# Optimization experiments

Measured on AMD Instinct MI355X. Metric: run time of the kernel, lower is better.

The kernel has to match this reference:

```python
import jax, jax.numpy as jnp
import numpy as np

B, SRC = 32, 1024
SEQ_LEN, CONTEXT_LEN, D_MODEL, VOCAB = 128, 5, 512, 32000


def setup_inputs() -> dict:
    key = jax.random.key(0)
    k1, k2, k3, k4, k5, k6 = jax.random.split(key, 6)
    x = jax.random.randint(k1, (B, SRC), 0, VOCAB, dtype=jnp.int64 if jax.config.jax_enable_x64 else jnp.int32)
    yc = jax.random.randint(k2, (B, SEQ_LEN * CONTEXT_LEN), 0, VOCAB, dtype=x.dtype)
    F_emb = jax.random.normal(k3, (VOCAB, D_MODEL), dtype=jnp.float32) * 0.02
    G_emb = jax.random.normal(k4, (VOCAB, D_MODEL), dtype=jnp.float32) * 0.02
    fan_in = CONTEXT_LEN * D_MODEL
    P_w = jax.random.uniform(k5, (fan_in, D_MODEL), dtype=jnp.float32,
                             minval=-1.0, maxval=1.0) * (fan_in ** -0.5)
    P_b = jnp.zeros((D_MODEL,), dtype=jnp.float32)
    return {"x": x, "yc": yc, "F_emb": F_emb, "G_emb": G_emb, "P_w": P_w, "P_b": P_b}


def reference(x, yc, F_emb, G_emb, P_w, P_b):
    # padding mask from source tokens: 1.0 where token == 0
    mask = (x == 0).astype(jnp.float32)                      # [B, SRC]
    xe = F_emb[x]                                            # [B, SRC, D]
    yce = G_emb[yc].reshape(-1, SEQ_LEN, CONTEXT_LEN * D_MODEL)  # [B, SEQ, C*D]
    py = jnp.einsum('bsk,kd->bsd', yce, P_w) + P_b           # Dense P(y): [B, SEQ, D]
    a = jnp.einsum('bxd,bsd->bxs', xe, py)                   # [B, SRC, SEQ]
    a = a + mask[:, :, None] * -1e9                          # mask padded source rows
    a = jnp.transpose(a, (0, 2, 1))                          # [B, SEQ, SRC]
    a = jax.nn.softmax(a, axis=-1)
    out = jnp.einsum('bsx,bxd->bsd', a, xe)                  # [B, SEQ, D]
    return (out, a)
```

## Files before the change

kernel.cpp:

```cpp
#include <hip/hip_runtime.h>
#include <hip/hip_bf16.h>
#include <stdint.h>

#define BATCH 32
#define SRCN 1024
#define SEQL 128
#define CTXN 5
#define DMOD 512

typedef __attribute__((ext_vector_type(8))) short short8;
typedef __attribute__((ext_vector_type(4))) float floatx4;

typedef __attribute__((address_space(3))) void lds_t;
typedef __attribute__((address_space(1))) void glb_t;

__device__ __forceinline__ void gload_lds16(const void* g, void* l) {
    __builtin_amdgcn_global_load_lds((const glb_t*)g, (lds_t*)l, 16, 0, 0);
}

__device__ __forceinline__ ushort f2b(float f) {
    __hip_bfloat16 h = __float2bfloat16(f);
    return *reinterpret_cast<ushort*>(&h);
}

#define LSLOT(m, sg) ((((m) << 3) | ((sg) ^ ((m) & 7))) << 3)

__global__ __launch_bounds__(256) void k_gather(
    const int* __restrict__ yc, const float* __restrict__ G,
    ushort* __restrict__ yce,
    const float* __restrict__ Pw, ushort* __restrict__ Pwt,
    const int* __restrict__ x, const float* __restrict__ F,
    ushort* __restrict__ xe, ushort* __restrict__ xet)
{
    __shared__ char smem[17408];
    const int tid = threadIdx.x;
    const int bid = blockIdx.x;
    if (bid < 4096) {
        const int r = bid;
        const int b = r >> 7, s = r & 127;
        for (int i = tid; i < 640; i += 256) {
            const int c = i >> 7;
            const int tok = yc[b * (SEQL * CTXN) + s * CTXN + c];
            const float4 v = *(const float4*)(G + (size_t)tok * DMOD + (i & 127) * 4);
            ushort4 o;
            o.x = f2b(v.x); o.y = f2b(v.y); o.z = f2b(v.z); o.w = f2b(v.w);
            *(ushort4*)(yce + (size_t)r * 2560 + i * 4) = o;
        }
    } else if (bid < 4416) {
        float* t = (float*)smem;
        const int id = bid - 4096;
        const int k0 = (id % 40) * 64, n0 = (id / 40) * 64;
        #pragma unroll
        for (int it = 0; it < 4; ++it) {
            const int c = tid + it * 256;
            const int kr = c >> 4, c4 = c & 15;
            const float4 v = *(const float4*)(Pw + (size_t)(k0 + kr) * DMOD + n0 + c4 * 4);
            t[kr * 68 + c4 * 4 + 0] = v.x; t[kr * 68 + c4 * 4 + 1] = v.y;
            t[kr * 68 + c4 * 4 + 2] = v.z; t[kr * 68 + c4 * 4 + 3] = v.w;
        }
        __syncthreads();
        #pragma unroll
        for (int it = 0; it < 2; ++it) {
            const int c = tid + it * 256;
            const int n = c >> 3, seg = c & 7;
            ushort4 o0, o1;
            o0.x = f2b(t[(seg * 8 + 0) * 68 + n]); o0.y = f2b(t[(seg * 8 + 1) * 68 + n]);
            o0.z = f2b(t[(seg * 8 + 2) * 68 + n]); o0.w = f2b(t[(seg * 8 + 3) * 68 + n]);
            o1.x = f2b(t[(seg * 8 + 4) * 68 + n]); o1.y = f2b(t[(seg * 8 + 5) * 68 + n]);
            o1.z = f2b(t[(seg * 8 + 6) * 68 + n]); o1.w = f2b(t[(seg * 8 + 7) * 68 + n]);
            ushort* dst = Pwt + (size_t)(n0 + n) * 2560 + k0 + seg * 8;
            *(ushort4*)dst = o0; *(ushort4*)(dst + 4) = o1;
        }
    } else {
        ushort* t = (ushort*)smem;
        const int id = bid - 4416;
        const int z = id >> 7;
        const int rem = id & 127;
        const int x0 = (rem & 15) * 64, d0 = (rem >> 4) * 64;
        #pragma unroll
        for (int it = 0; it < 4; ++it) {
            const int c = tid + it * 256;
            const int row = c >> 4, seg = c & 15;
            const int tok = x[z * SRCN + x0 + row];
            const float4 v = *(const float4*)(F + (size_t)tok * DMOD + d0 + seg * 4);
            ushort4 o;
            o.x = f2b(v.x); o.y = f2b(v.y); o.z = f2b(v.z); o.w = f2b(v.w);
            *(ushort4*)&t[row * 72 + seg * 4] = o;
            *(ushort4*)(xe + (size_t)(z * SRCN + x0 + row) * DMOD + d0 + seg * 4) = o;
        }
        __syncthreads();
        #pragma unroll
        for (int it = 0; it < 2; ++it) {
            const int c = tid + it * 256;
            const int d = c >> 3, seg = c & 7;
            ushort4 o0, o1;
            o0.x = t[(seg * 8 + 0) * 72 + d]; o0.y = t[(seg * 8 + 1) * 72 + d];
            o0.z = t[(seg * 8 + 2) * 72 + d]; o0.w = t[(seg * 8 + 3) * 72 + d];
            o1.x = t[(seg * 8 + 4) * 72 + d]; o1.y = t[(seg * 8 + 5) * 72 + d];
            o1.z = t[(seg * 8 + 6) * 72 + d]; o1.w = t[(seg * 8 + 7) * 72 + d];
            ushort* dst = xet + (size_t)(z * DMOD + d0 + d) * SRCN + x0 + seg * 8;
            *(ushort4*)dst = o0; *(ushort4*)(dst + 4) = o1;
        }
    }
}

__global__ __launch_bounds__(256) void k_gemm_py(
    const ushort* __restrict__ yce, const ushort* __restrict__ pwt,
    const float* __restrict__ Pb, ushort* __restrict__ py)
{
    __shared__ ushort As[2 * 8 * 512];
    __shared__ ushort Bs[2 * 8 * 512];
    const int f = blockIdx.x;
    const int wg = ((f & 7) << 6) | (f >> 3);
    const int m = wg >> 3, n = wg & 7;
    const int tid = threadIdx.x;
    const int w = tid >> 6, lane = tid & 63;
    const int l15 = lane & 15, q = lane >> 4;
    const int wm = w >> 1, wn = w & 1;
    const int m0 = m * 64, n0 = n * 64;

    const int sr = lane >> 3;
    const int ssg = ((lane & 7) ^ sr) * 8;

    const ushort* Abase = yce + (size_t)(m0 + sr) * 2560 + ssg;
    const ushort* Bbase = pwt + (size_t)(n0 + sr) * 2560 + ssg;

    floatx4 acc[2][2];
    #pragma unroll
    for (int mi = 0; mi < 2; ++mi)
        #pragma unroll
        for (int ni = 0; ni < 2; ++ni)
            acc[mi][ni] = (floatx4){0.f, 0.f, 0.f, 0.f};

    for (int kk = 0; kk < 2560; kk += 128) {
        __syncthreads();
        #pragma unroll
        for (int sub = 0; sub < 2; ++sub) {
            #pragma unroll
            for (int i = 0; i < 2; ++i) {
                const int cc = w * 2 + i;
                gload_lds16(Abase + (size_t)(cc * 8) * 2560 + kk + sub * 64,
                            (void*)(As + sub * 4096 + cc * 512));
                gload_lds16(Bbase + (size_t)(cc * 8) * 2560 + kk + sub * 64,
                            (void*)(Bs + sub * 4096 + cc * 512));
            }
        }
        __syncthreads();
        #pragma unroll
        for (int sub = 0; sub < 2; ++sub) {
            #pragma unroll
            for (int s2 = 0; s2 < 2; ++s2) {
                const int sg = s2 * 4 + q;
                short8 af[2], bf[2];
                #pragma unroll
                for (int mi = 0; mi < 2; ++mi)
                    af[mi] = *(const short8*)(As + sub * 4096 + LSLOT(wm * 32 + mi * 16 + l15, sg));
                #pragma unroll
                for (int ni = 0; ni < 2; ++ni)
                    bf[ni] = *(const short8*)(Bs + sub * 4096 + LSLOT(wn * 32 + ni * 16 + l15, sg));
                #pragma unroll
                for (int mi = 0; mi < 2; ++mi)
                    #pragma unroll
                    for (int ni = 0; ni < 2; ++ni)
                        acc[mi][ni] = __builtin_amdgcn_mfma_f32_16x16x32_bf16(
                            af[mi], bf[ni], acc[mi][ni], 0, 0, 0);
            }
        }
    }

    #pragma unroll
    for (int ni = 0; ni < 2; ++ni) {
        const int col = n0 + wn * 32 + ni * 16 + l15;
        const float bias = Pb[col];
        #pragma unroll
        for (int mi = 0; mi < 2; ++mi) {
            const int row0 = m0 + wm * 32 + mi * 16 + q * 4;
            #pragma unroll
            for (int r = 0; r < 4; ++r)
                py[(size_t)(row0 + r) * DMOD + col] = f2b(acc[mi][ni][r] + bias);
        }
    }
}

__global__ __launch_bounds__(256) void k_gemm_sc(
    const ushort* __restrict__ py, const int* __restrict__ x,
    const ushort* __restrict__ xe, float* __restrict__ a_out)
{
    __shared__ ushort As[16 * 512];
    __shared__ ushort Bs[8 * 512];
    const int f = blockIdx.x;
    const int g = f >> 3;
    const int b = ((g & 3) << 3) | (f & 7);
    const int n = g >> 2;
    const int tid = threadIdx.x;
    const int w = tid >> 6, lane = tid & 63;
    const int l15 = lane & 15, q = lane >> 4;
    const int wm = w >> 1, wn = w & 1;
    const int n0 = n * 64;

    const int sr = lane >> 3;
    const int ssg = ((lane & 7) ^ sr) * 8;

    const ushort* Abase = py + (size_t)(b * SEQL + sr) * DMOD + ssg;
    const ushort* Bbase = xe + (size_t)(b * SRCN + n0 + sr) * DMOD + ssg;

    floatx4 acc[4][2];
    #pragma unroll
    for (int mi = 0; mi < 4; ++mi)
        #pragma unroll
        for (int ni = 0; ni < 2; ++ni)
            acc[mi][ni] = (floatx4){0.f, 0.f, 0.f, 0.f};

    for (int kk = 0; kk < DMOD; kk += 64) {
        __syncthreads();
        #pragma unroll
        for (int i = 0; i < 4; ++i) {
            const int cc = w * 4 + i;
            gload_lds16(Abase + (size_t)(cc * 8) * DMOD + kk, (void*)(As + cc * 512));
        }
        #pragma unroll
        for (int i = 0; i < 2; ++i) {
            const int cc = w * 2 + i;
            gload_lds16(Bbase + (size_t)(cc * 8) * DMOD + kk, (void*)(Bs + cc * 512));
        }
        __syncthreads();
        #pragma unroll
        for (int s2 = 0; s2 < 2; ++s2) {
            const int sg = s2 * 4 + q;
            short8 af[4], bf[2];
            #pragma unroll
            for (int mi = 0; mi < 4; ++mi)
                af[mi] = *(const short8*)(As + LSLOT(wm * 64 + mi * 16 + l15, sg));
            #pragma unroll
            for (int ni = 0; ni < 2; ++ni)
                bf[ni] = *(const short8*)(Bs + LSLOT(wn * 32 + ni * 16 + l15, sg));
            #pragma unroll
            for (int mi = 0; mi < 4; ++mi)
                #pragma unroll
                for (int ni = 0; ni < 2; ++ni)
                    acc[mi][ni] = __builtin_amdgcn_mfma_f32_16x16x32_bf16(
                        af[mi], bf[ni], acc[mi][ni], 0, 0, 0);
        }
    }

    #pragma unroll
    for (int ni = 0; ni < 2; ++ni) {
        const int col = n0 + wn * 32 + ni * 16 + l15;
        const float msk = (x[b * SRCN + col] == 0) ? -1e9f : 0.0f;
        #pragma unroll
        for (int mi = 0; mi < 4; ++mi) {
            const int row0 = wm * 64 + mi * 16 + q * 4;
            #pragma unroll
            for (int r = 0; r < 4; ++r)
                a_out[((size_t)b * SEQL + row0 + r) * SRCN + col] = acc[mi][ni][r] + msk;
        }
    }
}

__global__ __launch_bounds__(256) void k_softmax(
    float* __restrict__ a, ushort* __restrict__ abf)
{
    const int row = blockIdx.x;
    float* p = a + (size_t)row * SRCN;
    ushort* pb = abf + (size_t)row * SRCN;
    const int tid = threadIdx.x;
    const int wave = tid >> 6, lane = tid & 63;

    float4 v = *(const float4*)(p + tid * 4);

    float mx = fmaxf(fmaxf(v.x, v.y), fmaxf(v.z, v.w));
    #pragma unroll
    for (int off = 32; off > 0; off >>= 1)
        mx = fmaxf(mx, __shfl_down(mx, off, 64));
    __shared__ float redm[4];
    if (lane == 0) redm[wave] = mx;
    __syncthreads();
    mx = fmaxf(fmaxf(redm[0], redm[1]), fmaxf(redm[2], redm[3]));

    const float e0 = __expf(v.x - mx);
    const float e1 = __expf(v.y - mx);
    const float e2 = __expf(v.z - mx);
    const float e3 = __expf(v.w - mx);

    float sm = e0 + e1 + e2 + e3;
    #pragma unroll
    for (int off = 32; off > 0; off >>= 1)
        sm += __shfl_down(sm, off, 64);
    __shared__ float reds[4];
    if (lane == 0) reds[wave] = sm;
    __syncthreads();
    sm = reds[0] + reds[1] + reds[2] + reds[3];

    const float inv = 1.0f / sm;
    float4 o;
    o.x = e0 * inv; o.y = e1 * inv; o.z = e2 * inv; o.w = e3 * inv;
    *(float4*)(p + tid * 4) = o;
    ushort4 ob;
    ob.x = f2b(o.x); ob.y = f2b(o.y); ob.z = f2b(o.z); ob.w = f2b(o.w);
    *(ushort4*)(pb + tid * 4) = ob;
}

__global__ __launch_bounds__(256) void k_gemm_out(
    const ushort* __restrict__ abf, const ushort* __restrict__ xet,
    float* __restrict__ outp)
{
    __shared__ ushort As[2 * 8 * 512];
    __shared__ ushort Bs[2 * 8 * 512];
    const int f = blockIdx.x;
    const int g = f >> 3;
    const int b = ((g & 3) << 3) | (f & 7);
    const int h = g >> 2;
    const int m = h & 1, n = h >> 1;
    const int tid = threadIdx.x;
    const int w = tid >> 6, lane = tid & 63;
    const int l15 = lane & 15, q = lane >> 4;
    const int wm = w >> 1, wn = w & 1;
    const int m0 = m * 64, n0 = n * 64;

    const int sr = lane >> 3;
    const int ssg = ((lane & 7) ^ sr) * 8;

    const ushort* Abase = abf + (size_t)(b * SEQL + m0 + sr) * SRCN + ssg;
    const ushort* Bbase = xet + (size_t)(b * DMOD + n0 + sr) * SRCN + ssg;

    floatx4 acc[2][2];
    #pragma unroll
    for (int mi = 0; mi < 2; ++mi)
        #pragma unroll
        for (int ni = 0; ni < 2; ++ni)
            acc[mi][ni] = (floatx4){0.f, 0.f, 0.f, 0.f};

    for (int kk = 0; kk < SRCN; kk += 128) {
        __syncthreads();
        #pragma unroll
        for (int sub = 0; sub < 2; ++sub) {
            #pragma unroll
            for (int i = 0; i < 2; ++i) {
                const int cc = w * 2 + i;
                gload_lds16(Abase + (size_t)(cc * 8) * SRCN + kk + sub * 64,
                            (void*)(As + sub * 4096 + cc * 512));
                gload_lds16(Bbase + (size_t)(cc * 8) * SRCN + kk + sub * 64,
                            (void*)(Bs + sub * 4096 + cc * 512));
            }
        }
        __syncthreads();
        #pragma unroll
        for (int sub = 0; sub < 2; ++sub) {
            #pragma unroll
            for (int s2 = 0; s2 < 2; ++s2) {
                const int sg = s2 * 4 + q;
                short8 af[2], bf[2];
                #pragma unroll
                for (int mi = 0; mi < 2; ++mi)
                    af[mi] = *(const short8*)(As + sub * 4096 + LSLOT(wm * 32 + mi * 16 + l15, sg));
                #pragma unroll
                for (int ni = 0; ni < 2; ++ni)
                    bf[ni] = *(const short8*)(Bs + sub * 4096 + LSLOT(wn * 32 + ni * 16 + l15, sg));
                #pragma unroll
                for (int mi = 0; mi < 2; ++mi)
                    #pragma unroll
                    for (int ni = 0; ni < 2; ++ni)
                        acc[mi][ni] = __builtin_amdgcn_mfma_f32_16x16x32_bf16(
                            af[mi], bf[ni], acc[mi][ni], 0, 0, 0);
            }
        }
    }

    #pragma unroll
    for (int ni = 0; ni < 2; ++ni) {
        const int col = n0 + wn * 32 + ni * 16 + l15;
        #pragma unroll
        for (int mi = 0; mi < 2; ++mi) {
            const int row0 = m0 + wm * 32 + mi * 16 + q * 4;
            #pragma unroll
            for (int r = 0; r < 4; ++r)
                outp[((size_t)b * SEQL + row0 + r) * DMOD + col] = acc[mi][ni][r];
        }
    }
}

extern "C" void kernel_launch(void* const* d_in, const int* in_sizes, int n_in,
                              void* d_out, int out_size, void* d_ws, size_t ws_size,
                              hipStream_t stream)
{
    const int*   x    = (const int*)d_in[0];
    const int*   yc   = (const int*)d_in[1];
    const float* Femb = (const float*)d_in[2];
    const float* Gemb = (const float*)d_in[3];
    const float* Pw   = (const float*)d_in[4];
    const float* Pb   = (const float*)d_in[5];

    float* out_p = (float*)d_out;
    float* a_p   = out_p + (size_t)BATCH * SEQL * DMOD;

    char* ws = (char*)d_ws;
    ushort* yce  = (ushort*)(ws);
    ushort* abf  = (ushort*)(ws);
    ushort* pwt  = (ushort*)(ws + 20971520);
    ushort* xe   = (ushort*)(ws + 23592960);
    ushort* xet  = (ushort*)(ws + 57147392);
    ushort* py   = (ushort*)(ws + 90701824);

    dim3 blk(256);
    k_gather<<<dim3(8512), blk, 0, stream>>>(yc, Gemb, yce, Pw, pwt, x, Femb, xe, xet);

    k_gemm_py<<<dim3(512), blk, 0, stream>>>(yce, pwt, Pb, py);

    k_gemm_sc<<<dim3(512), blk, 0, stream>>>(py, x, xe, a_p);
    k_softmax<<<dim3(4096), blk, 0, stream>>>(a_p, abf);
    k_gemm_out<<<dim3(512), blk, 0, stream>>>(abf, xet, out_p);
}
```

Baseline: 211.7 us.

## Overlap x-embedding gather/transposes with the py GEMM in one launch

Splits the gather kernel so the x-embedding gather and transpose run in the same launch as the py GEMM blocks, letting the two independent stages overlap on the device instead of running back to back. Token indices are staged once into shared memory instead of being reloaded per thread. LDS row strides are changed to reduce bank conflicts in the transposes. The GEMM blocks now share a launch with many gather blocks, which can shift occupancy and scheduling.

```diff
diff --git a/kernel.cpp b/kernel.cpp
--- a/kernel.cpp
+++ b/kernel.cpp
@@ -25,29 +25,32 @@
 
 #define LSLOT(m, sg) ((((m) << 3) | ((sg) ^ ((m) & 7))) << 3)
 
-__global__ __launch_bounds__(256) void k_gather(
+#define XSTR 74
+#define PSTR 69
+
+__global__ __launch_bounds__(256) void k_gather_y(
     const int* __restrict__ yc, const float* __restrict__ G,
     ushort* __restrict__ yce,
-    const float* __restrict__ Pw, ushort* __restrict__ Pwt,
-    const int* __restrict__ x, const float* __restrict__ F,
-    ushort* __restrict__ xe, ushort* __restrict__ xet)
-{
-    __shared__ char smem[17408];
+    const float* __restrict__ Pw, ushort* __restrict__ Pwt)
+{
+    __shared__ float tf[64 * PSTR];
     const int tid = threadIdx.x;
     const int bid = blockIdx.x;
     if (bid < 4096) {
+        int* toks = (int*)tf;
         const int r = bid;
         const int b = r >> 7, s = r & 127;
+        if (tid < CTXN) toks[tid] = yc[b * (SEQL * CTXN) + s * CTXN + tid];
+        __syncthreads();
         for (int i = tid; i < 640; i += 256) {
             const int c = i >> 7;
-            const int tok = yc[b * (SEQL * CTXN) + s * CTXN + c];
+            const int tok = toks[c];
             const float4 v = *(const float4*)(G + (size_t)tok * DMOD + (i & 127) * 4);
             ushort4 o;
             o.x = f2b(v.x); o.y = f2b(v.y); o.z = f2b(v.z); o.w = f2b(v.w);
             *(ushort4*)(yce + (size_t)r * 2560 + i * 4) = o;
         }
-    } else if (bid < 4416) {
-        float* t = (float*)smem;
+    } else {
         const int id = bid - 4096;
         const int k0 = (id % 40) * 64, n0 = (id / 40) * 64;
         #pragma unroll
@@ -55,8 +58,8 @@
             const int c = tid + it * 256;
             const int kr = c >> 4, c4 = c & 15;
             const float4 v = *(const float4*)(Pw + (size_t)(k0 + kr) * DMOD + n0 + c4 * 4);
-            t[kr * 68 + c4 * 4 + 0] = v.x; t[kr * 68 + c4 * 4 + 1] = v.y;
-            t[kr * 68 + c4 * 4 + 2] = v.z; t[kr * 68 + c4 * 4 + 3] = v.w;
+            tf[kr * PSTR + c4 * 4 + 0] = v.x; tf[kr * PSTR + c4 * 4 + 1] = v.y;
+            tf[kr * PSTR + c4 * 4 + 2] = v.z; tf[kr * PSTR + c4 * 4 + 3] = v.w;
         }
         __syncthreads();
         #pragma unroll
@@ -64,28 +67,116 @@
             const int c = tid + it * 256;
             const int n = c >> 3, seg = c & 7;
             ushort4 o0, o1;
-            o0.x = f2b(t[(seg * 8 + 0) * 68 + n]); o0.y = f2b(t[(seg * 8 + 1) * 68 + n]);
-            o0.z = f2b(t[(seg * 8 + 2) * 68 + n]); o0.w = f2b(t[(seg * 8 + 3) * 68 + n]);
-            o1.x = f2b(t[(seg * 8 + 4) * 68 + n]); o1.y = f2b(t[(seg * 8 + 5) * 68 + n]);
-            o1.z = f2b(t[(seg * 8 + 6) * 68 + n]); o1.w = f2b(t[(seg * 8 + 7) * 68 + n]);
+            o0.x = f2b(tf[(seg * 8 + 0) * PSTR + n]); o0.y = f2b(tf[(seg * 8 + 1) * PSTR + n]);
+            o0.z = f2b(tf[(seg * 8 + 2) * PSTR + n]); o0.w = f2b(tf[(seg * 8 + 3) * PSTR + n]);
+            o1.x = f2b(tf[(seg * 8 + 4) * PSTR + n]); o1.y = f2b(tf[(seg * 8 + 5) * PSTR + n]);
+            o1.z = f2b(tf[(seg * 8 + 6) * PSTR + n]); o1.w = f2b(tf[(seg * 8 + 7) * PSTR + n]);
             ushort* dst = Pwt + (size_t)(n0 + n) * 2560 + k0 + seg * 8;
             *(ushort4*)dst = o0; *(ushort4*)(dst + 4) = o1;
         }
+    }
+}
+
+__global__ __launch_bounds__(256) void k_pyx(
+    const ushort* __restrict__ yce, const ushort* __restrict__ pwt,
+    const float* __restrict__ Pb, ushort* __restrict__ py,
+    const int* __restrict__ x, const float* __restrict__ F,
+    ushort* __restrict__ xe, ushort* __restrict__ xet)
+{
+    __shared__ ushort smem[16384];
+    const int tid = threadIdx.x;
+    const int bid = blockIdx.x;
+
+    if (bid < 512) {
+        ushort* As = smem;
+        ushort* Bs = smem + 8192;
+        const int f = bid;
+        const int wg = ((f & 7) << 6) | (f >> 3);
+        const int m = wg >> 3, n = wg & 7;
+        const int w = tid >> 6, lane = tid & 63;
+        const int l15 = lane & 15, q = lane >> 4;
+        const int wm = w >> 1, wn = w & 1;
+        const int m0 = m * 64, n0 = n * 64;
+
+        const int sr = lane >> 3;
+        const int ssg = ((lane & 7) ^ sr) * 8;
+
+        const ushort* Abase = yce + (size_t)(m0 + sr) * 2560 + ssg;
+        const ushort* Bbase = pwt + (size_t)(n0 + sr) * 2560 + ssg;
+
+        floatx4 acc[2][2];
+        #pragma unroll
+        for (int mi = 0; mi < 2; ++mi)
+            #pragma unroll
+            for (int ni = 0; ni < 2; ++ni)
+                acc[mi][ni] = (floatx4){0.f, 0.f, 0.f, 0.f};
+
+        for (int kk = 0; kk < 2560; kk += 128) {
+            __syncthreads();
+            #pragma unroll
+            for (int sub = 0; sub < 2; ++sub) {
+                #pragma unroll
+                for (int i = 0; i < 2; ++i) {
+                    const int cc = w * 2 + i;
+                    gload_lds16(Abase + (size_t)(cc * 8) * 2560 + kk + sub * 64,
+                                (void*)(As + sub * 4096 + cc * 512));
+                    gload_lds16(Bbase + (size_t)(cc * 8) * 2560 + kk + sub * 64,
+                                (void*)(Bs + sub * 4096 + cc * 512));
+                }
+            }
+            __syncthreads();
+            #pragma unroll
+            for (int sub = 0; sub < 2; ++sub) {
+                #pragma unroll
+                for (int s2 = 0; s2 < 2; ++s2) {
+                    const int sg = s2 * 4 + q;
+                    short8 af[2], bf[2];
+                    #pragma unroll
+                    for (int mi = 0; mi < 2; ++mi)
+                        af[mi] = *(const short8*)(As + sub * 4096 + LSLOT(wm * 32 + mi * 16 + l15, sg));
+                    #pragma unroll
+                    for (int ni = 0; ni < 2; ++ni)
+                        bf[ni] = *(const short8*)(Bs + sub * 4096 + LSLOT(wn * 32 + ni * 16 + l15, sg));
+                    #pragma unroll
+                    for (int mi = 0; mi < 2; ++mi)
+                        #pragma unroll
+                        for (int ni = 0; ni < 2; ++ni)
+                            acc[mi][ni] = __builtin_amdgcn_mfma_f32_16x16x32_bf16(
+                                af[mi], bf[ni], acc[mi][ni], 0, 0, 0);
+                }
+            }
+        }
+
+        #pragma unroll
+        for (int ni = 0; ni < 2; ++ni) {
+            const int col = n0 + wn * 32 + ni * 16 + l15;
+            const float bias = Pb[col];
+            #pragma unroll
+            for (int mi = 0; mi < 2; ++mi) {
+                const int row0 = m0 + wm * 32 + mi * 16 + q * 4;
+                #pragma unroll
+                for (int r = 0; r < 4; ++r)
+                    py[(size_t)(row0 + r) * DMOD + col] = f2b(acc[mi][ni][r] + bias);
+            }
+        }
     } else {
-        ushort* t = (ushort*)smem;
-        const int id = bid - 4416;
+        ushort* t = smem;
+        int* toks = (int*)(smem + 64 * XSTR);
+        const int id = bid - 512;
         const int z = id >> 7;
         const int rem = id & 127;
         const int x0 = (rem & 15) * 64, d0 = (rem >> 4) * 64;
+        if (tid < 64) toks[tid] = x[z * SRCN + x0 + tid];
+        __syncthreads();
         #pragma unroll
         for (int it = 0; it < 4; ++it) {
             const int c = tid + it * 256;
             const int row = c >> 4, seg = c & 15;
-            const int tok = x[z * SRCN + x0 + row];
+            const int tok = toks[row];
             const float4 v = *(const float4*)(F + (size_t)tok * DMOD + d0 + seg * 4);
             ushort4 o;
             o.x = f2b(v.x); o.y = f2b(v.y); o.z = f2b(v.z); o.w = f2b(v.w);
-            *(ushort4*)&t[row * 72 + seg * 4] = o;
+            *(ushort4*)&t[row * XSTR + seg * 4] = o;
             *(ushort4*)(xe + (size_t)(z * SRCN + x0 + row) * DMOD + d0 + seg * 4) = o;
         }
         __syncthreads();
@@ -94,90 +185,12 @@
             const int c = tid + it * 256;
             const int d = c >> 3, seg = c & 7;
             ushort4 o0, o1;
-            o0.x = t[(seg * 8 + 0) * 72 + d]; o0.y = t[(seg * 8 + 1) * 72 + d];
-            o0.z = t[(seg * 8 + 2) * 72 + d]; o0.w = t[(seg * 8 + 3) * 72 + d];
-            o1.x = t[(seg * 8 + 4) * 72 + d]; o1.y = t[(seg * 8 + 5) * 72 + d];
-            o1.z = t[(seg * 8 + 6) * 72 + d]; o1.w = t[(seg * 8 + 7) * 72 + d];
+            o0.x = t[(seg * 8 + 0) * XSTR + d]; o0.y = t[(seg * 8 + 1) * XSTR + d];
+            o0.z = t[(seg * 8 + 2) * XSTR + d]; o0.w = t[(seg * 8 + 3) * XSTR + d];
+            o1.x = t[(seg * 8 + 4) * XSTR + d]; o1.y = t[(seg * 8 + 5) * XSTR + d];
+            o1.z = t[(seg * 8 + 6) * XSTR + d]; o1.w = t[(seg * 8 + 7) * XSTR + d];
             ushort* dst = xet + (size_t)(z * DMOD + d0 + d) * SRCN + x0 + seg * 8;
             *(ushort4*)dst = o0; *(ushort4*)(dst + 4) = o1;
-        }
-    }
-}
-
-__global__ __launch_bounds__(256) void k_gemm_py(
-    const ushort* __restrict__ yce, const ushort* __restrict__ pwt,
-    const float* __restrict__ Pb, ushort* __restrict__ py)
-{
-    __shared__ ushort As[2 * 8 * 512];
-    __shared__ ushort Bs[2 * 8 * 512];
-    const int f = blockIdx.x;
-    const int wg = ((f & 7) << 6) | (f >> 3);
-    const int m = wg >> 3, n = wg & 7;
-    const int tid = threadIdx.x;
-    const int w = tid >> 6, lane = tid & 63;
-    const int l15 = lane & 15, q = lane >> 4;
-    const int wm = w >> 1, wn = w & 1;
-    const int m0 = m * 64, n0 = n * 64;
-
-    const int sr = lane >> 3;
-    const int ssg = ((lane & 7) ^ sr) * 8;
-
-    const ushort* Abase = yce + (size_t)(m0 + sr) * 2560 + ssg;
-    const ushort* Bbase = pwt + (size_t)(n0 + sr) * 2560 + ssg;
-
-    floatx4 acc[2][2];
-    #pragma unroll
-    for (int mi = 0; mi < 2; ++mi)
-        #pragma unroll
-        for (int ni = 0; ni < 2; ++ni)
-            acc[mi][ni] = (floatx4){0.f, 0.f, 0.f, 0.f};
-
-    for (int kk = 0; kk < 2560; kk += 128) {
-        __syncthreads();
-        #pragma unroll
-        for (int sub = 0; sub < 2; ++sub) {
-            #pragma unroll
-            for (int i = 0; i < 2; ++i) {
-                const int cc = w * 2 + i;
-                gload_lds16(Abase + (size_t)(cc * 8) * 2560 + kk + sub * 64,
-                            (void*)(As + sub * 4096 + cc * 512));
-                gload_lds16(Bbase + (size_t)(cc * 8) * 2560 + kk + sub * 64,
-                            (void*)(Bs + sub * 4096 + cc * 512));
-            }
-        }
-        __syncthreads();
-        #pragma unroll
-        for (int sub = 0; sub < 2; ++sub) {
-            #pragma unroll
-            for (int s2 = 0; s2 < 2; ++s2) {
-                const int sg = s2 * 4 + q;
-                short8 af[2], bf[2];
-                #pragma unroll
-                for (int mi = 0; mi < 2; ++mi)
-                    af[mi] = *(const short8*)(As + sub * 4096 + LSLOT(wm * 32 + mi * 16 + l15, sg));
-                #pragma unroll
-                for (int ni = 0; ni < 2; ++ni)
-                    bf[ni] = *(const short8*)(Bs + sub * 4096 + LSLOT(wn * 32 + ni * 16 + l15, sg));
-                #pragma unroll
-                for (int mi = 0; mi < 2; ++mi)
-                    #pragma unroll
-                    for (int ni = 0; ni < 2; ++ni)
-                        acc[mi][ni] = __builtin_amdgcn_mfma_f32_16x16x32_bf16(
-                            af[mi], bf[ni], acc[mi][ni], 0, 0, 0);
-            }
-        }
-    }
-
-    #pragma unroll
-    for (int ni = 0; ni < 2; ++ni) {
-        const int col = n0 + wn * 32 + ni * 16 + l15;
-        const float bias = Pb[col];
-        #pragma unroll
-        for (int mi = 0; mi < 2; ++mi) {
-            const int row0 = m0 + wm * 32 + mi * 16 + q * 4;
-            #pragma unroll
-            for (int r = 0; r < 4; ++r)
-                py[(size_t)(row0 + r) * DMOD + col] = f2b(acc[mi][ni][r] + bias);
         }
     }
 }
@@ -402,9 +415,9 @@
     ushort* py   = (ushort*)(ws + 90701824);
 
     dim3 blk(256);
-    k_gather<<<dim3(8512), blk, 0, stream>>>(yc, Gemb, yce, Pw, pwt, x, Femb, xe, xet);
-
-    k_gemm_py<<<dim3(512), blk, 0, stream>>>(yce, pwt, Pb, py);
+    k_gather_y<<<dim3(4416), blk, 0, stream>>>(yc, Gemb, yce, Pw, pwt);
+
+    k_pyx<<<dim3(4608), blk, 0, stream>>>(yce, pwt, Pb, py, x, Femb, xe, xet);
 
     k_gemm_sc<<<dim3(512), blk, 0, stream>>>(py, x, xe, a_p);
     k_softmax<<<dim3(4096), blk, 0, stream>>>(a_p, abf);
```

After: 217.9 us. 1.03x slower.

## Fuse softmax into output GEMM, recomputing probabilities on the fly

Applied to the files above, without the earlier changes.

Removes the separate softmax kernel. The score GEMM now writes raw masked scores to workspace, and the attention-output kernel makes two passes per row to find max and sum. It then recomputes exp-normalized probabilities per K tile, packs them to bf16 in LDS, and has only n==0 blocks write the fp32 attention matrix. This saves one launch and the bf16 probability round trip, but each of the 8 column blocks rereads the raw score rows three times and redoes the exponentials, and the K tile shrinks to 64.

```diff
diff --git a/kernel.cpp b/kernel.cpp
--- a/kernel.cpp
+++ b/kernel.cpp
@@ -184,7 +184,7 @@
 
 __global__ __launch_bounds__(256) void k_gemm_sc(
     const ushort* __restrict__ py, const int* __restrict__ x,
-    const ushort* __restrict__ xe, float* __restrict__ a_out)
+    const ushort* __restrict__ xe, float* __restrict__ sraw)
 {
     __shared__ ushort As[16 * 512];
     __shared__ ushort Bs[8 * 512];
@@ -252,60 +252,18 @@
             const int row0 = wm * 64 + mi * 16 + q * 4;
             #pragma unroll
             for (int r = 0; r < 4; ++r)
-                a_out[((size_t)b * SEQL + row0 + r) * SRCN + col] = acc[mi][ni][r] + msk;
-        }
-    }
-}
-
-__global__ __launch_bounds__(256) void k_softmax(
-    float* __restrict__ a, ushort* __restrict__ abf)
+                sraw[((size_t)b * SEQL + row0 + r) * SRCN + col] = acc[mi][ni][r] + msk;
+        }
+    }
+}
+
+__global__ __launch_bounds__(256) void k_att(
+    const float* __restrict__ sraw, const ushort* __restrict__ xet,
+    float* __restrict__ a_out, float* __restrict__ outp)
 {
-    const int row = blockIdx.x;
-    float* p = a + (size_t)row * SRCN;
-    ushort* pb = abf + (size_t)row * SRCN;
-    const int tid = threadIdx.x;
-    const int wave = tid >> 6, lane = tid & 63;
-
-    float4 v = *(const float4*)(p + tid * 4);
-
-    float mx = fmaxf(fmaxf(v.x, v.y), fmaxf(v.z, v.w));
-    #pragma unroll
-    for (int off = 32; off > 0; off >>= 1)
-        mx = fmaxf(mx, __shfl_down(mx, off, 64));
-    __shared__ float redm[4];
-    if (lane == 0) redm[wave] = mx;
-    __syncthreads();
-    mx = fmaxf(fmaxf(redm[0], redm[1]), fmaxf(redm[2], redm[3]));
-
-    const float e0 = __expf(v.x - mx);
-    const float e1 = __expf(v.y - mx);
-    const float e2 = __expf(v.z - mx);
-    const float e3 = __expf(v.w - mx);
-
-    float sm = e0 + e1 + e2 + e3;
-    #pragma unroll
-    for (int off = 32; off > 0; off >>= 1)
-        sm += __shfl_down(sm, off, 64);
-    __shared__ float reds[4];
-    if (lane == 0) reds[wave] = sm;
-    __syncthreads();
-    sm = reds[0] + reds[1] + reds[2] + reds[3];
-
-    const float inv = 1.0f / sm;
-    float4 o;
-    o.x = e0 * inv; o.y = e1 * inv; o.z = e2 * inv; o.w = e3 * inv;
-    *(float4*)(p + tid * 4) = o;
-    ushort4 ob;
-    ob.x = f2b(o.x); ob.y = f2b(o.y); ob.z = f2b(o.z); ob.w = f2b(o.w);
-    *(ushort4*)(pb + tid * 4) = ob;
-}
-
-__global__ __launch_bounds__(256) void k_gemm_out(
-    const ushort* __restrict__ abf, const ushort* __restrict__ xet,
-    float* __restrict__ outp)
-{
-    __shared__ ushort As[2 * 8 * 512];
-    __shared__ ushort Bs[2 * 8 * 512];
+    __shared__ ushort As[8 * 512];
+    __shared__ ushort Bs[8 * 512];
+    __shared__ float smx[64], sinv[64];
     const int f = blockIdx.x;
     const int g = f >> 3;
     const int b = ((g & 3) << 3) | (f & 7);
@@ -317,10 +275,33 @@
     const int wm = w >> 1, wn = w & 1;
     const int m0 = m * 64, n0 = n * 64;
 
+    const int prow = tid >> 2, pj = tid & 3;
+    const float* srow = sraw + ((size_t)b * SEQL + m0 + prow) * SRCN;
+    float mx = -3.0e38f;
+    for (int k = 0; k < 64; ++k) {
+        const float4 v = *(const float4*)(srow + (size_t)(k * 4 + pj) * 4);
+        mx = fmaxf(mx, fmaxf(fmaxf(v.x, v.y), fmaxf(v.z, v.w)));
+    }
+    mx = fmaxf(mx, __shfl_xor(mx, 1, 64));
+    mx = fmaxf(mx, __shfl_xor(mx, 2, 64));
+    float sm = 0.f;
+    for (int k = 0; k < 64; ++k) {
+        const float4 v = *(const float4*)(srow + (size_t)(k * 4 + pj) * 4);
+        sm += __expf(v.x - mx) + __expf(v.y - mx) + __expf(v.z - mx) + __expf(v.w - mx);
+    }
+    sm += __shfl_xor(sm, 1, 64);
+    sm += __shfl_xor(sm, 2, 64);
+    if (pj == 0) { smx[prow] = mx; sinv[prow] = 1.0f / sm; }
+    __syncthreads();
+
+    const int arow = tid >> 2;
+    const int sp = (tid & 3) * 2;
+    const float amx = smx[arow], ainv = sinv[arow];
+    const float* srow2 = sraw + ((size_t)b * SEQL + m0 + arow) * SRCN;
+    float* arow_out = a_out + ((size_t)b * SEQL + m0 + arow) * SRCN;
+
     const int sr = lane >> 3;
     const int ssg = ((lane & 7) ^ sr) * 8;
-
-    const ushort* Abase = abf + (size_t)(b * SEQL + m0 + sr) * SRCN + ssg;
     const ushort* Bbase = xet + (size_t)(b * DMOD + n0 + sr) * SRCN + ssg;
 
     floatx4 acc[2][2];
@@ -330,39 +311,53 @@
         for (int ni = 0; ni < 2; ++ni)
             acc[mi][ni] = (floatx4){0.f, 0.f, 0.f, 0.f};
 
-    for (int kk = 0; kk < SRCN; kk += 128) {
-        __syncthreads();
-        #pragma unroll
-        for (int sub = 0; sub < 2; ++sub) {
-            #pragma unroll
-            for (int i = 0; i < 2; ++i) {
-                const int cc = w * 2 + i;
-                gload_lds16(Abase + (size_t)(cc * 8) * SRCN + kk + sub * 64,
-                            (void*)(As + sub * 4096 + cc * 512));
-                gload_lds16(Bbase + (size_t)(cc * 8) * SRCN + kk + sub * 64,
-                            (void*)(Bs + sub * 4096 + cc * 512));
+    for (int kk = 0; kk < SRCN; kk += 64) {
+        __syncthreads();
+        #pragma unroll
+        for (int i = 0; i < 2; ++i) {
+            const int cc = w * 2 + i;
+            gload_lds16(Bbase + (size_t)(cc * 8) * SRCN + kk, (void*)(Bs + cc * 512));
+        }
+        #pragma unroll
+        for (int ss = 0; ss < 2; ++ss) {
+            const int seg = sp + ss;
+            const float4 v0 = *(const float4*)(srow2 + kk + seg * 8);
+            const float4 v1 = *(const float4*)(srow2 + kk + seg * 8 + 4);
+            float p0 = __expf(v0.x - amx) * ainv, p1 = __expf(v0.y - amx) * ainv;
+            float p2 = __expf(v0.z - amx) * ainv, p3 = __expf(v0.w - amx) * ainv;
+            float p4 = __expf(v1.x - amx) * ainv, p5 = __expf(v1.y - amx) * ainv;
+            float p6 = __expf(v1.z - amx) * ainv, p7 = __expf(v1.w - amx) * ainv;
+            short8 pk;
+            pk[0] = (short)f2b(p0); pk[1] = (short)f2b(p1);
+            pk[2] = (short)f2b(p2); pk[3] = (short)f2b(p3);
+            pk[4] = (short)f2b(p4); pk[5] = (short)f2b(p5);
+            pk[6] = (short)f2b(p6); pk[7] = (short)f2b(p7);
+            *(short8*)(As + LSLOT(arow, seg)) = pk;
+            if (n == 0) {
+                float4 o0, o1;
+                o0.x = p0; o0.y = p1; o0.z = p2; o0.w = p3;
+                o1.x = p4; o1.y = p5; o1.z = p6; o1.w = p7;
+                *(float4*)(arow_out + kk + seg * 8) = o0;
+                *(float4*)(arow_out + kk + seg * 8 + 4) = o1;
             }
         }
         __syncthreads();
         #pragma unroll
-        for (int sub = 0; sub < 2; ++sub) {
-            #pragma unroll
-            for (int s2 = 0; s2 < 2; ++s2) {
-                const int sg = s2 * 4 + q;
-                short8 af[2], bf[2];
-                #pragma unroll
-                for (int mi = 0; mi < 2; ++mi)
-                    af[mi] = *(const short8*)(As + sub * 4096 + LSLOT(wm * 32 + mi * 16 + l15, sg));
+        for (int s2 = 0; s2 < 2; ++s2) {
+            const int sg = s2 * 4 + q;
+            short8 af[2], bf[2];
+            #pragma unroll
+            for (int mi = 0; mi < 2; ++mi)
+                af[mi] = *(const short8*)(As + LSLOT(wm * 32 + mi * 16 + l15, sg));
+            #pragma unroll
+            for (int ni = 0; ni < 2; ++ni)
+                bf[ni] = *(const short8*)(Bs + LSLOT(wn * 32 + ni * 16 + l15, sg));
+            #pragma unroll
+            for (int mi = 0; mi < 2; ++mi)
                 #pragma unroll
                 for (int ni = 0; ni < 2; ++ni)
-                    bf[ni] = *(const short8*)(Bs + sub * 4096 + LSLOT(wn * 32 + ni * 16 + l15, sg));
-                #pragma unroll
-                for (int mi = 0; mi < 2; ++mi)
-                    #pragma unroll
-                    for (int ni = 0; ni < 2; ++ni)
-                        acc[mi][ni] = __builtin_amdgcn_mfma_f32_16x16x32_bf16(
-                            af[mi], bf[ni], acc[mi][ni], 0, 0, 0);
-            }
+                    acc[mi][ni] = __builtin_amdgcn_mfma_f32_16x16x32_bf16(
+                        af[mi], bf[ni], acc[mi][ni], 0, 0, 0);
         }
     }
 
@@ -395,7 +390,7 @@
 
     char* ws = (char*)d_ws;
     ushort* yce  = (ushort*)(ws);
-    ushort* abf  = (ushort*)(ws);
+    float*  sraw = (float*)(ws);
     ushort* pwt  = (ushort*)(ws + 20971520);
     ushort* xe   = (ushort*)(ws + 23592960);
     ushort* xet  = (ushort*)(ws + 57147392);
@@ -406,7 +401,7 @@
 
     k_gemm_py<<<dim3(512), blk, 0, stream>>>(yce, pwt, Pb, py);
 
-    k_gemm_sc<<<dim3(512), blk, 0, stream>>>(py, x, xe, a_p);
-    k_softmax<<<dim3(4096), blk, 0, stream>>>(a_p, abf);
-    k_gemm_out<<<dim3(512), blk, 0, stream>>>(abf, xet, out_p);
-}
+    k_gemm_sc<<<dim3(512), blk, 0, stream>>>(py, x, xe, sraw);
+
+    k_att<<<dim3(512), blk, 0, stream>>>(sraw, xet, a_p, out_p);
+}
```

Result: slower. 235.9 us (+11.4%).
